# Kernel tuning notes

Measured on AMD Instinct MI355X. Metric: run time of the kernel, lower is better.

The kernel has to match this reference:

```python
import jax, jax.numpy as jnp
import numpy as np

BS, N_GENES, N_FEAT = 4, 15135, 64
HIDDEN, NUM_LAYERS = 128, 2
HIDDEN_FC, N_CMT, N_CLASSES = 256, 1000, 10
N_EDGES = 100000


def _linear_params(k, din, dout):
    # torch.nn.Linear default init: U(-1/sqrt(din), 1/sqrt(din))
    s = 1.0 / np.sqrt(din)
    kw, kb = jax.random.split(k)
    W = jax.random.uniform(kw, (din, dout), jnp.float32, -s, s)
    b = jax.random.uniform(kb, (dout,), jnp.float32, -s, s)
    return W, b


def setup_inputs() -> dict:
    key = jax.random.key(0)
    ks = jax.random.split(key, 9)
    W1, b1 = _linear_params(ks[0], N_FEAT, HIDDEN)
    W2, b2 = _linear_params(ks[1], HIDDEN, HIDDEN)
    Wfc, bfc = _linear_params(ks[2], NUM_LAYERS * HIDDEN, 1)
    Wl1, bl1 = _linear_params(ks[3], N_CMT, HIDDEN_FC)
    Wl2, bl2 = _linear_params(ks[4], HIDDEN_FC, N_CLASSES)
    x = jax.random.normal(ks[5], (BS, N_GENES, N_FEAT), jnp.float32)
    row = jax.random.randint(ks[6], (N_EDGES,), 0, N_GENES)
    col = jax.random.randint(ks[7], (N_EDGES,), 0, N_CMT)
    batch = jnp.zeros((BS,), jnp.int32)  # accepted but unused by forward
    return dict(x=x, batch=batch, row=row, col=col,
                W1=W1, b1=b1, W2=W2, b2=b2, Wfc=Wfc, bfc=bfc,
                Wl1=Wl1, bl1=bl1, Wl2=Wl2, bl2=bl2)


def reference(x, batch, row, col, W1, b1, W2, b2, Wfc, bfc, Wl1, bl1, Wl2, bl2):
    bs, n = x.shape[0], x.shape[1]
    # MLP stack (mode='cat', no batchnorm)
    h1 = jax.nn.relu(jnp.einsum('bnf,fh->bnh', x, W1) + b1)   # [bs, n, H]
    h2 = jax.nn.relu(jnp.einsum('bnh,hk->bnk', h1, W2) + b2)  # [bs, n, H]
    # torch.stack(xs, -1).view(bs, n, -1): layers interleaved per hidden unit
    feat = jnp.stack([h1, h2], axis=-1).reshape(bs, n, -1)    # [bs, n, 2H]
    # pathway pooling: gather nodes by row, segment-mean into n_cmt groups
    g = jnp.transpose(feat, (1, 0, 2))[row]                   # [E, bs, 2H]
    seg_sum = jax.ops.segment_sum(g, col, num_segments=N_CMT)          # [n_cmt, bs, 2H]
    cnt = jax.ops.segment_sum(jnp.ones_like(col, feat.dtype), col,
                              num_segments=N_CMT)                      # [n_cmt]
    seg_mean = seg_sum / jnp.maximum(cnt, 1.0)[:, None, None]          # empty segs -> 0
    pooled = jnp.transpose(seg_mean, (1, 0, 2)).reshape(-1, feat.shape[-1])  # [bs*n_cmt, 2H]
    scores = (pooled @ Wfc + bfc).reshape(-1, N_CMT)          # [bs, n_cmt]
    # head (eval mode: dropout is identity)
    h = jax.nn.relu(scores @ Wl1 + bl1)                       # [bs, hidden_fc]
    logits = h @ Wl2 + bl2                                    # [bs, n_classes]
    return jax.nn.log_softmax(logits, axis=-1)
```

## Files before the change

kernel.cpp:

```cpp
#include <hip/hip_runtime.h>
#include <hip/hip_bf16.h>

#define BSZ   4
#define NG    15135
#define MROWS (BSZ*NG)
#define NF    64
#define H     128
#define NCMT  1000
#define NEDGE 100000
#define HFC   256
#define NCLS  10
#define NB2   128
#define CCH   25

typedef __attribute__((ext_vector_type(8))) short  bfrag;
typedef __attribute__((ext_vector_type(4))) float  f32x4;

__device__ __forceinline__ unsigned int pkbf(float a, float b) {
    union { __hip_bfloat162 h2; unsigned int u; } c;
    c.h2 = __float22bfloat162_rn(make_float2(a, b));
    return c.u;
}

__global__ __launch_bounds__(256) void kP(const float* __restrict__ W1,
                                          const float* __restrict__ W2,
                                          const float* __restrict__ bl1,
                                          unsigned int* __restrict__ wfrag_u32,
                                          float* __restrict__ hacc,
                                          float* __restrict__ acc,
                                          int* __restrict__ cnt) {
    const int q = blockIdx.x * 256 + threadIdx.x;
    if (q < BSZ * HFC) hacc[q] = bl1[q & (HFC - 1)];
    if (q < BSZ * NCMT) acc[q] = 0.f;
    if (q < NCMT)       cnt[q] = 0;

    const int e = 2 * q;
    float f0, f1;
    if (e < 8192) {
        const int kk = e & 7, l = (e >> 3) & 63, ct = e >> 9;
        const int t = ct & 1, ci = ct >> 1;
        const int k = t * 32 + (l >> 4) * 8 + kk;
        const int i = ci * 16 + (l & 15);
        f0 = W1[k * H + i];
        f1 = W1[(k + 1) * H + i];
    } else {
        const int e2 = e - 8192;
        const int kk = e2 & 7, l = (e2 >> 3) & 63, ct = e2 >> 9;
        const int t = ct & 3, ci = ct >> 2;
        const int k = t * 32 + (l >> 4) * 8 + kk;
        const int i = ci * 16 + (l & 15);
        f0 = W2[k * H + i];
        f1 = W2[(k + 1) * H + i];
    }
    wfrag_u32[q] = pkbf(f0, f1);
}

__global__ __launch_bounds__(256, 2) void k1_fdot(const float* __restrict__ x,
                                                  const unsigned int* __restrict__ wfrag_g,
                                                  const float* __restrict__ b1,
                                                  const float* __restrict__ b2,
                                                  const float* __restrict__ Wfc,
                                                  float* __restrict__ fdot4) {
    __shared__ unsigned int   wfrag[12288];
    __shared__ unsigned short h1s[4][16][136];

    const int tid  = threadIdx.x;
    const int lane = tid & 63, wid = tid >> 6;
    const int sub  = lane & 15, grp = lane >> 4;
    const int r  = blockIdx.x * 64 + wid * 16 + sub;
    const int rc = r < MROWS ? r : MROWS - 1;

    float4 xr[4];
    #pragma unroll
    for (int t = 0; t < 2; ++t) {
        xr[2 * t]     = *(const float4*)&x[(size_t)rc * NF + t * 32 + grp * 8];
        xr[2 * t + 1] = *(const float4*)&x[(size_t)rc * NF + t * 32 + grp * 8 + 4];
    }

    {
        const uint4* src = (const uint4*)wfrag_g;
        uint4* dst = (uint4*)wfrag;
        #pragma unroll
        for (int i = 0; i < 12; ++i) dst[i * 256 + tid] = src[i * 256 + tid];
    }
    __syncthreads();

    bfrag bx[2];
    #pragma unroll
    for (int t = 0; t < 2; ++t) {
        union { bfrag v; unsigned int u[4]; } pk;
        const float4 a = xr[2 * t], b = xr[2 * t + 1];
        pk.u[0] = pkbf(a.x, a.y); pk.u[1] = pkbf(a.z, a.w);
        pk.u[2] = pkbf(b.x, b.y); pk.u[3] = pkbf(b.z, b.w);
        bx[t] = pk.v;
    }

    const bfrag* w1f = (const bfrag*)wfrag;
    const bfrag* w2f = (const bfrag*)(wfrag + 4096);
    float fp = 0.f;

    #pragma unroll
    for (int ci = 0; ci < 8; ++ci) {
        f32x4 c1 = {0.f, 0.f, 0.f, 0.f};
        c1 = __builtin_amdgcn_mfma_f32_16x16x32_bf16(w1f[(ci * 2 + 0) * 64 + lane], bx[0], c1, 0, 0, 0);
        c1 = __builtin_amdgcn_mfma_f32_16x16x32_bf16(w1f[(ci * 2 + 1) * 64 + lane], bx[1], c1, 0, 0, 0);
        const int c0 = ci * 16 + grp * 4;
        const float4 b1v = *(const float4*)&b1[c0];
        const float4 wfa = *(const float4*)&Wfc[2 * c0];
        const float4 wfb = *(const float4*)&Wfc[2 * c0 + 4];
        const float h0 = fmaxf(c1[0] + b1v.x, 0.f);
        const float h1 = fmaxf(c1[1] + b1v.y, 0.f);
        const float h2 = fmaxf(c1[2] + b1v.z, 0.f);
        const float h3 = fmaxf(c1[3] + b1v.w, 0.f);
        fp = fmaf(h0, wfa.x, fp); fp = fmaf(h1, wfa.z, fp);
        fp = fmaf(h2, wfb.x, fp); fp = fmaf(h3, wfb.z, fp);
        *(uint2*)&h1s[wid][sub][c0] = make_uint2(pkbf(h0, h1), pkbf(h2, h3));
    }

    bfrag bh[4];
    #pragma unroll
    for (int t = 0; t < 4; ++t)
        bh[t] = *(const bfrag*)&h1s[wid][sub][t * 32 + grp * 8];

    #pragma unroll
    for (int ci = 0; ci < 8; ++ci) {
        f32x4 c2 = {0.f, 0.f, 0.f, 0.f};
        #pragma unroll
        for (int t = 0; t < 4; ++t)
            c2 = __builtin_amdgcn_mfma_f32_16x16x32_bf16(w2f[(ci * 4 + t) * 64 + lane], bh[t], c2, 0, 0, 0);
        const int c0 = ci * 16 + grp * 4;
        const float4 b2v = *(const float4*)&b2[c0];
        const float4 wfa = *(const float4*)&Wfc[2 * c0];
        const float4 wfb = *(const float4*)&Wfc[2 * c0 + 4];
        fp = fmaf(fmaxf(c2[0] + b2v.x, 0.f), wfa.y, fp);
        fp = fmaf(fmaxf(c2[1] + b2v.y, 0.f), wfa.w, fp);
        fp = fmaf(fmaxf(c2[2] + b2v.z, 0.f), wfb.y, fp);
        fp = fmaf(fmaxf(c2[3] + b2v.w, 0.f), wfb.w, fp);
    }

    fp += __shfl_xor(fp, 16);
    fp += __shfl_xor(fp, 32);
    if (grp == 0 && r < MROWS) {
        const int b = r / NG, g = r - b * NG;
        fdot4[g * 4 + b] = fp;
    }
}

__global__ __launch_bounds__(512) void k2_scatter(const int* __restrict__ row,
                                                  const int* __restrict__ col,
                                                  const float* __restrict__ fdot4,
                                                  float* __restrict__ acc,
                                                  int* __restrict__ cnt) {
    __shared__ float lacc[4 * NCMT];
    __shared__ int   lcnt[NCMT];
    const int tid = threadIdx.x;

    for (int i = tid; i < 4 * NCMT; i += 512) lacc[i] = 0.f;
    for (int i = tid; i < NCMT; i += 512) lcnt[i] = 0;
    __syncthreads();

    for (int e = blockIdx.x * 512 + tid; e < NEDGE; e += NB2 * 512) {
        const int r = row[e];
        const int c = col[e];
        const float4 f = *(const float4*)&fdot4[r * 4];
        unsafeAtomicAdd(&lacc[c],            f.x);
        unsafeAtomicAdd(&lacc[NCMT + c],     f.y);
        unsafeAtomicAdd(&lacc[2 * NCMT + c], f.z);
        unsafeAtomicAdd(&lacc[3 * NCMT + c], f.w);
        atomicAdd(&lcnt[c], 1);
    }
    __syncthreads();

    for (int i = tid; i < 4 * NCMT; i += 512)
        unsafeAtomicAdd(&acc[i], lacc[i]);
    for (int i = tid; i < NCMT; i += 512)
        atomicAdd(&cnt[i], lcnt[i]);
}

__global__ __launch_bounds__(256) void k3a_head1(const float* __restrict__ acc,
                                                 const int* __restrict__ cnt,
                                                 const float* __restrict__ bfc,
                                                 const float* __restrict__ Wl1,
                                                 float* __restrict__ hacc) {
    __shared__ float sc[BSZ][CCH];
    const int c0 = blockIdx.x * CCH;
    const int t = threadIdx.x;

    if (t < BSZ * CCH) {
        const int b = t / CCH, cc = t % CCH;
        const int c = c0 + cc;
        sc[b][cc] = acc[b * NCMT + c] / fmaxf((float)cnt[c], 1.f) + bfc[0];
    }
    __syncthreads();

    float p0 = 0.f, p1 = 0.f, p2 = 0.f, p3 = 0.f;
    #pragma unroll
    for (int cc = 0; cc < CCH; ++cc) {
        const float wv = Wl1[(size_t)(c0 + cc) * HFC + t];
        p0 = fmaf(sc[0][cc], wv, p0);
        p1 = fmaf(sc[1][cc], wv, p1);
        p2 = fmaf(sc[2][cc], wv, p2);
        p3 = fmaf(sc[3][cc], wv, p3);
    }
    unsafeAtomicAdd(&hacc[0 * HFC + t], p0);
    unsafeAtomicAdd(&hacc[1 * HFC + t], p1);
    unsafeAtomicAdd(&hacc[2 * HFC + t], p2);
    unsafeAtomicAdd(&hacc[3 * HFC + t], p3);
}

__global__ __launch_bounds__(256) void k3b_head2(const float* __restrict__ hacc,
                                                 const float* __restrict__ Wl2,
                                                 const float* __restrict__ bl2,
                                                 float* __restrict__ out) {
    __shared__ float wl2s[HFC][NCLS + 2];
    __shared__ float hr[BSZ][HFC + 4];
    __shared__ float part[BSZ][NCLS][6];
    __shared__ float lg[BSZ][NCLS];
    const int t = threadIdx.x;

    #pragma unroll
    for (int i = t; i < HFC * NCLS; i += 256)
        wl2s[i / NCLS][i % NCLS] = Wl2[i];
    #pragma unroll
    for (int q = 0; q < BSZ; ++q)
        hr[q][t] = fmaxf(hacc[q * HFC + t], 0.f);
    __syncthreads();

    if (t < BSZ * NCLS * 6) {
        const int b = t / (NCLS * 6), rem = t % (NCLS * 6);
        const int k = rem / 6, ch = rem % 6;
        const int j0 = ch * 43;
        const int j1 = (j0 + 43 > HFC) ? HFC : j0 + 43;
        float p = 0.f;
        for (int j = j0; j < j1; ++j)
            p = fmaf(hr[b][j], wl2s[j][k], p);
        part[b][k][ch] = p;
    }
    __syncthreads();

    if (t < BSZ * NCLS) {
        const int b = t / NCLS, k = t % NCLS;
        float a = bl2[k];
        #pragma unroll
        for (int ch = 0; ch < 6; ++ch) a += part[b][k][ch];
        lg[b][k] = a;
    }
    __syncthreads();
    if (t < BSZ * NCLS) {
        const int b = t / NCLS, k = t % NCLS;
        float m = lg[b][0];
        #pragma unroll
        for (int k2 = 1; k2 < NCLS; ++k2) m = fmaxf(m, lg[b][k2]);
        float s = 0.f;
        #pragma unroll
        for (int k2 = 0; k2 < NCLS; ++k2) s += expf(lg[b][k2] - m);
        out[b * NCLS + k] = lg[b][k] - m - logf(s);
    }
}

extern "C" void kernel_launch(void* const* d_in, const int* in_sizes, int n_in,
                              void* d_out, int out_size, void* d_ws, size_t ws_size,
                              hipStream_t stream) {
    const float* x   = (const float*)d_in[0];
    const int*   row = (const int*)d_in[2];
    const int*   col = (const int*)d_in[3];
    const float* W1  = (const float*)d_in[4];
    const float* b1  = (const float*)d_in[5];
    const float* W2  = (const float*)d_in[6];
    const float* b2  = (const float*)d_in[7];
    const float* Wfc = (const float*)d_in[8];
    const float* bfc = (const float*)d_in[9];
    const float* Wl1 = (const float*)d_in[10];
    const float* bl1 = (const float*)d_in[11];
    const float* Wl2 = (const float*)d_in[12];
    const float* bl2 = (const float*)d_in[13];

    float* ws    = (float*)d_ws;
    float* fdot4 = ws;
    float* acc   = ws + 60544;
    int*   cnt   = (int*)(ws + 64544);
    float* hacc  = ws + 65544;
    unsigned int* wfrag = (unsigned int*)(ws + 66568);

    kP<<<48, 256, 0, stream>>>(W1, W2, bl1, wfrag, hacc, acc, cnt);
    k1_fdot<<<(MROWS + 63) / 64, 256, 0, stream>>>(x, wfrag, b1, b2, Wfc, fdot4);
    k2_scatter<<<NB2, 512, 0, stream>>>(row, col, fdot4, acc, cnt);
    k3a_head1<<<NCMT / CCH, 256, 0, stream>>>(acc, cnt, bfc, Wl1, hacc);
    k3b_head2<<<1, 256, 0, stream>>>(hacc, Wl2, bl2, (float*)d_out);
}
```

Baseline: 36.59 us.

## Fold weight-packing prep kernel into k1 and widen scatter blocks

Removes the separate prep kernel. Each k1 block now reads W1/W2 from global memory, converts them to bf16 and writes them straight into shared memory in MFMA fragment order. The first 16 blocks also zero the accumulators and seed hacc with bl1. k2_scatter switches to 64 blocks of 1024 threads, so fewer block-level partial sums are merged with global atomics. This saves one launch but makes every k1 block (about 950) redo the fp32 weight transpose and conversion with strided global reads, which may lengthen k1's prologue.

```diff
diff --git a/kernel.cpp b/kernel.cpp
--- a/kernel.cpp
+++ b/kernel.cpp
@@ -10,7 +10,7 @@
 #define NEDGE 100000
 #define HFC   256
 #define NCLS  10
-#define NB2   128
+#define NB2   64
 #define CCH   25
 
 typedef __attribute__((ext_vector_type(8))) short  bfrag;
@@ -22,45 +22,17 @@
     return c.u;
 }
 
-__global__ __launch_bounds__(256) void kP(const float* __restrict__ W1,
-                                          const float* __restrict__ W2,
-                                          const float* __restrict__ bl1,
-                                          unsigned int* __restrict__ wfrag_u32,
-                                          float* __restrict__ hacc,
-                                          float* __restrict__ acc,
-                                          int* __restrict__ cnt) {
-    const int q = blockIdx.x * 256 + threadIdx.x;
-    if (q < BSZ * HFC) hacc[q] = bl1[q & (HFC - 1)];
-    if (q < BSZ * NCMT) acc[q] = 0.f;
-    if (q < NCMT)       cnt[q] = 0;
-
-    const int e = 2 * q;
-    float f0, f1;
-    if (e < 8192) {
-        const int kk = e & 7, l = (e >> 3) & 63, ct = e >> 9;
-        const int t = ct & 1, ci = ct >> 1;
-        const int k = t * 32 + (l >> 4) * 8 + kk;
-        const int i = ci * 16 + (l & 15);
-        f0 = W1[k * H + i];
-        f1 = W1[(k + 1) * H + i];
-    } else {
-        const int e2 = e - 8192;
-        const int kk = e2 & 7, l = (e2 >> 3) & 63, ct = e2 >> 9;
-        const int t = ct & 3, ci = ct >> 2;
-        const int k = t * 32 + (l >> 4) * 8 + kk;
-        const int i = ci * 16 + (l & 15);
-        f0 = W2[k * H + i];
-        f1 = W2[(k + 1) * H + i];
-    }
-    wfrag_u32[q] = pkbf(f0, f1);
-}
-
 __global__ __launch_bounds__(256, 2) void k1_fdot(const float* __restrict__ x,
-                                                  const unsigned int* __restrict__ wfrag_g,
+                                                  const float* __restrict__ W1,
+                                                  const float* __restrict__ W2,
                                                   const float* __restrict__ b1,
                                                   const float* __restrict__ b2,
                                                   const float* __restrict__ Wfc,
-                                                  float* __restrict__ fdot4) {
+                                                  const float* __restrict__ bl1,
+                                                  float* __restrict__ fdot4,
+                                                  float* __restrict__ acc,
+                                                  int* __restrict__ cnt,
+                                                  float* __restrict__ hacc) {
     __shared__ unsigned int   wfrag[12288];
     __shared__ unsigned short h1s[4][16][136];
 
@@ -77,11 +49,32 @@
         xr[2 * t + 1] = *(const float4*)&x[(size_t)rc * NF + t * 32 + grp * 8 + 4];
     }
 
-    {
-        const uint4* src = (const uint4*)wfrag_g;
-        uint4* dst = (uint4*)wfrag;
-        #pragma unroll
-        for (int i = 0; i < 12; ++i) dst[i * 256 + tid] = src[i * 256 + tid];
+    if (blockIdx.x < 16) {
+        const int q = blockIdx.x * 256 + tid;
+        if (q < BSZ * NCMT) acc[q] = 0.f;
+        if (q < NCMT)       cnt[q] = 0;
+        if (q < BSZ * HFC)  hacc[q] = bl1[q & (HFC - 1)];
+    }
+
+    #pragma unroll
+    for (int it = 0; it < 16; ++it) {
+        const int m = it * 256 + tid;
+        const int i = m & 127, k = (m >> 7) * 2;
+        const float f0 = W1[k * H + i];
+        const float f1 = W1[(k + 1) * H + i];
+        const int S = (((i >> 4) * 2 + (k >> 5)) * 64 + ((k >> 3) & 3) * 16 + (i & 15)) * 4
+                      + ((k & 7) >> 1);
+        wfrag[S] = pkbf(f0, f1);
+    }
+    #pragma unroll
+    for (int it = 0; it < 32; ++it) {
+        const int m = it * 256 + tid;
+        const int i = m & 127, k = (m >> 7) * 2;
+        const float f0 = W2[k * H + i];
+        const float f1 = W2[(k + 1) * H + i];
+        const int S = (((i >> 4) * 4 + (k >> 5)) * 64 + ((k >> 3) & 3) * 16 + (i & 15)) * 4
+                      + ((k & 7) >> 1) + 4096;
+        wfrag[S] = pkbf(f0, f1);
     }
     __syncthreads();
 
@@ -146,20 +139,20 @@
     }
 }
 
-__global__ __launch_bounds__(512) void k2_scatter(const int* __restrict__ row,
-                                                  const int* __restrict__ col,
-                                                  const float* __restrict__ fdot4,
-                                                  float* __restrict__ acc,
-                                                  int* __restrict__ cnt) {
+__global__ __launch_bounds__(1024) void k2_scatter(const int* __restrict__ row,
+                                                   const int* __restrict__ col,
+                                                   const float* __restrict__ fdot4,
+                                                   float* __restrict__ acc,
+                                                   int* __restrict__ cnt) {
     __shared__ float lacc[4 * NCMT];
     __shared__ int   lcnt[NCMT];
     const int tid = threadIdx.x;
 
-    for (int i = tid; i < 4 * NCMT; i += 512) lacc[i] = 0.f;
-    for (int i = tid; i < NCMT; i += 512) lcnt[i] = 0;
-    __syncthreads();
-
-    for (int e = blockIdx.x * 512 + tid; e < NEDGE; e += NB2 * 512) {
+    for (int i = tid; i < 4 * NCMT; i += 1024) lacc[i] = 0.f;
+    for (int i = tid; i < NCMT; i += 1024) lcnt[i] = 0;
+    __syncthreads();
+
+    for (int e = blockIdx.x * 1024 + tid; e < NEDGE; e += NB2 * 1024) {
         const int r = row[e];
         const int c = col[e];
         const float4 f = *(const float4*)&fdot4[r * 4];
@@ -171,9 +164,9 @@
     }
     __syncthreads();
 
-    for (int i = tid; i < 4 * NCMT; i += 512)
+    for (int i = tid; i < 4 * NCMT; i += 1024)
         unsafeAtomicAdd(&acc[i], lacc[i]);
-    for (int i = tid; i < NCMT; i += 512)
+    for (int i = tid; i < NCMT; i += 1024)
         atomicAdd(&cnt[i], lcnt[i]);
 }
 
@@ -280,11 +273,10 @@
     float* acc   = ws + 60544;
     int*   cnt   = (int*)(ws + 64544);
     float* hacc  = ws + 65544;
-    unsigned int* wfrag = (unsigned int*)(ws + 66568);
-
-    kP<<<48, 256, 0, stream>>>(W1, W2, bl1, wfrag, hacc, acc, cnt);
-    k1_fdot<<<(MROWS + 63) / 64, 256, 0, stream>>>(x, wfrag, b1, b2, Wfc, fdot4);
-    k2_scatter<<<NB2, 512, 0, stream>>>(row, col, fdot4, acc, cnt);
+
+    k1_fdot<<<(MROWS + 63) / 64, 256, 0, stream>>>(x, W1, W2, b1, b2, Wfc, bl1,
+                                                   fdot4, acc, cnt, hacc);
+    k2_scatter<<<NB2, 1024, 0, stream>>>(row, col, fdot4, acc, cnt);
     k3a_head1<<<NCMT / CCH, 256, 0, stream>>>(acc, cnt, bfc, Wl1, hacc);
     k3b_head2<<<1, 256, 0, stream>>>(hacc, Wl2, bl2, (float*)d_out);
 }
```

After: 38.25 us. +4.5%, slower.
